# Optimization experiments

Measured on AMD Instinct MI355X. Metric: run time of the kernel, lower is better.

Reference implementation:

```python
import jax, jax.numpy as jnp
import numpy as np
import math

B, S, D, H = 4, 2048, 1024, 16
DK = D // H


def _rope_tables(seq_len, dim, dtype=jnp.float32):
    inv_freq = 1.0 / (10000.0 ** (jnp.arange(0, dim, 2, dtype=jnp.float32) / dim))
    t = jnp.arange(seq_len, dtype=jnp.float32)
    freqs = jnp.einsum('i,j->ij', t, inv_freq)          # [S, dim/2]
    emb = jnp.concatenate([freqs, freqs], axis=-1)       # [S, dim]
    return jnp.cos(emb).astype(dtype)[None, None], jnp.sin(emb).astype(dtype)[None, None]


def _apply_rope(x, cos, sin):
    # faithful to source: rotated = cat([-x[...,1::2], x[...,::2]], -1)
    x_rot = jnp.concatenate([-x[..., 1::2], x[..., ::2]], axis=-1)
    return x * cos + x_rot * sin


def setup_inputs() -> dict:
    key = jax.random.key(0)
    ks = jax.random.split(key, 12)
    scale = 1.0 / math.sqrt(D)
    inp = {
        'query': jax.random.normal(ks[0], (B, S, D), jnp.float32),
        'key':   jax.random.normal(ks[1], (B, S, D), jnp.float32),
        'value': jax.random.normal(ks[2], (B, S, D), jnp.float32),
        'mask':  jnp.tril(jnp.ones((S, S), jnp.int32))[None, None],  # causal [1,1,S,S]
        'w_q': jax.random.normal(ks[3], (D, D), jnp.float32) * scale,
        'b_q': jnp.zeros((D,), jnp.float32),
        'w_k': jax.random.normal(ks[4], (D, D), jnp.float32) * scale,
        'b_k': jnp.zeros((D,), jnp.float32),
        'w_v': jax.random.normal(ks[5], (D, D), jnp.float32) * scale,
        'b_v': jnp.zeros((D,), jnp.float32),
        'w_o': jax.random.normal(ks[6], (D, D), jnp.float32) * scale,
        'b_o': jnp.zeros((D,), jnp.float32),
    }
    return inp


def reference(query, key, value, mask, w_q, b_q, w_k, b_k, w_v, b_v, w_o, b_o):
    b, s, _ = query.shape
    # projections (torch Linear: x @ W.T + b), split heads -> [B,H,S,Dk]
    def proj(x, w, bias):
        return (x @ w.T + bias).reshape(b, -1, H, DK).transpose(0, 2, 1, 3)
    Q = proj(query, w_q, b_q)
    K = proj(key, w_k, b_k)
    V = proj(value, w_v, b_v)
    cos, sin = _rope_tables(s, DK, Q.dtype)
    Q = _apply_rope(Q, cos, sin)
    K = _apply_rope(K, cos, sin)
    scores = jnp.einsum('bhqd,bhkd->bhqk', Q, K) / math.sqrt(DK)
    scores = jnp.where(mask == 0, jnp.asarray(-1e9, scores.dtype), scores)
    attn = jax.nn.softmax(scores, axis=-1)
    ctx = jnp.einsum('bhqk,bhkd->bhqd', attn, V)
    ctx = ctx.transpose(0, 2, 1, 3).reshape(b, -1, D)
    return ctx @ w_o.T + b_o
```

## Files before the change

### kernel.cpp

```cpp
#include <hip/hip_runtime.h>
#include <hip/hip_bf16.h>
#include <math.h>

#define B_  4
#define S_  2048
#define D_  1024
#define H_  16
#define DK_ 64
#define M_  (B_ * S_)

typedef short short8 __attribute__((ext_vector_type(8)));
typedef float floatx4 __attribute__((ext_vector_type(4)));

__device__ inline unsigned short f2bf(float x) {
    unsigned u = __float_as_uint(x);
    u = (u + 0x7fff + ((u >> 16) & 1)) >> 16;
    return (unsigned short)u;
}
__device__ inline float bf2f(unsigned short h) {
    return __uint_as_float(((unsigned)h) << 16);
}

__device__ inline unsigned cvt_pk_bf16(float lo, float hi) {
    unsigned r;
    asm("v_cvt_pk_bf16_f32 %0, %1, %2" : "=v"(r) : "v"(lo), "v"(hi));
    return r;
}

template <int K>
__device__ inline float dpp_ror(float x) {
    return __uint_as_float((unsigned)__builtin_amdgcn_update_dpp(
        0, (int)__float_as_uint(x), 0x120 | K, 0xF, 0xF, true));
}
__device__ inline float rowmax16(float x) {
    x = fmaxf(x, dpp_ror<8>(x));
    x = fmaxf(x, dpp_ror<4>(x));
    x = fmaxf(x, dpp_ror<2>(x));
    x = fmaxf(x, dpp_ror<1>(x));
    return x;
}
__device__ inline float rowsum16(float x) {
    x += dpp_ror<8>(x);
    x += dpp_ror<4>(x);
    x += dpp_ror<2>(x);
    x += dpp_ror<1>(x);
    return x;
}

#define GLOAD_LDS16(g, l)                                          \
    __builtin_amdgcn_global_load_lds(                              \
        (const __attribute__((address_space(1))) void*)(g),        \
        (__attribute__((address_space(3))) void*)(l), 16, 0, 0)

__global__ __launch_bounds__(256) void cvt_inputs_kernel(
    const float* __restrict__ q, const float* __restrict__ k,
    const float* __restrict__ v, unsigned short* __restrict__ Ah)
{
    const int z = blockIdx.z;
    const float* src = (z == 0) ? q : (z == 1) ? k : v;
    unsigned short* dst = Ah + (size_t)z * M_ * D_;
    const size_t i = ((size_t)blockIdx.x * 256 + threadIdx.x) * 4;
    float4 f = *(const float4*)(src + i);
    ushort4 o;
    o.x = f2bf(f.x); o.y = f2bf(f.y); o.z = f2bf(f.z); o.w = f2bf(f.w);
    *(ushort4*)(dst + i) = o;
}

__global__ __launch_bounds__(256) void cvt_weights_kernel(
    const float* __restrict__ wq, const float* __restrict__ wk,
    const float* __restrict__ wv, const float* __restrict__ wo,
    unsigned short* __restrict__ Wh, unsigned short* __restrict__ Woh)
{
    const int z = blockIdx.z;
    const float* src = (z == 0) ? wq : (z == 1) ? wk : (z == 2) ? wv : wo;
    unsigned short* dst = (z < 3) ? (Wh + (size_t)z * D_ * D_) : Woh;
    const size_t i = ((size_t)blockIdx.x * 256 + threadIdx.x) * 4;
    float4 f = *(const float4*)(src + i);
    ushort4 o;
    o.x = f2bf(f.x); o.y = f2bf(f.y); o.z = f2bf(f.z); o.w = f2bf(f.w);
    *(ushort4*)(dst + i) = o;
}

template <int MODE>
__global__ __launch_bounds__(256) void gemm_bf16_kernel(
    const unsigned short* __restrict__ Ah, const unsigned short* __restrict__ Wh,
    const float* __restrict__ bq, const float* __restrict__ bk,
    const float* __restrict__ bv, void* __restrict__ outv)
{
    __shared__ __align__(16) unsigned short As[128 * 32];
    __shared__ __align__(16) unsigned short Bs[128 * 32];
    __shared__ __align__(16) unsigned short Ts[MODE == 1 ? 4 * 16 * 68 : 4];

    const int tid  = threadIdx.x;
    const int wave = tid >> 6;
    const int lane = tid & 63;
    const int quad = lane >> 4;
    const int l15  = lane & 15;
    const int z    = (MODE == 1) ? blockIdx.z : 0;
    const int m0   = blockIdx.x * 128;
    const int n0   = blockIdx.y * 128;
    const int wrow = (wave >> 1) * 64;
    const int wcol = (wave & 1) * 64;

    const unsigned short* A = Ah + (size_t)z * M_ * D_;
    const unsigned short* W = Wh + (size_t)z * D_ * D_;

    const int srow   = tid >> 2;
    const int schunk = (tid & 3) * 8;

    floatx4 acc[4][4] = {};

    for (int k0 = 0; k0 < D_; k0 += 32) {
        __syncthreads();
#pragma unroll
        for (int p = 0; p < 2; ++p) {
            const unsigned short* ga =
                A + (size_t)(m0 + p * 64 + srow) * D_ + k0 + schunk;
            GLOAD_LDS16(ga, &As[p * 2048 + wave * 512]);
            const unsigned short* gb =
                W + (size_t)(n0 + p * 64 + srow) * D_ + k0 + schunk;
            GLOAD_LDS16(gb, &Bs[p * 2048 + wave * 512]);
        }
        __syncthreads();

        short8 af[4], bf[4];
#pragma unroll
        for (int i = 0; i < 4; ++i)
            af[i] = *(const short8*)&As[(wrow + i * 16 + l15) * 32 + quad * 8];
#pragma unroll
        for (int j = 0; j < 4; ++j)
            bf[j] = *(const short8*)&Bs[(wcol + j * 16 + l15) * 32 + quad * 8];
#pragma unroll
        for (int i = 0; i < 4; ++i)
#pragma unroll
            for (int j = 0; j < 4; ++j)
                acc[i][j] = __builtin_amdgcn_mfma_f32_16x16x32_bf16(
                    af[i], bf[j], acc[i][j], 0, 0, 0);
    }

    const float* bias = (MODE == 0) ? bq : (z == 0) ? bq : (z == 1) ? bk : bv;

    if (MODE == 1 && z == 2) {
        __syncthreads();
        unsigned short* Tw = &Ts[wave * 16 * 68];
        const int bgl = m0 >> 11;
        const int s0g = (m0 & (S_ - 1)) + wrow + quad * 16;
#pragma unroll
        for (int j = 0; j < 4; ++j) {
            const int n = n0 + wcol + j * 16 + l15;
            const float bn = bias[n];
#pragma unroll
            for (int i = 0; i < 4; ++i)
#pragma unroll
                for (int reg = 0; reg < 4; ++reg)
                    Tw[l15 * 68 + i * 16 + quad * 4 + reg] =
                        f2bf(acc[i][j][reg] + bn);
            short8 r0 = *(const short8*)&Tw[l15 * 68 + quad * 16];
            short8 r1 = *(const short8*)&Tw[l15 * 68 + quad * 16 + 8];
            const int h = n >> 6, d = n & 63;
            unsigned short* dp = (unsigned short*)outv + 2 * (size_t)M_ * D_ +
                (((size_t)(bgl * H_ + h)) * DK_ + d) * S_ + s0g;
            *(short8*)(dp) = r0;
            *(short8*)(dp + 8) = r1;
        }
        return;
    }

#pragma unroll
    for (int j = 0; j < 4; ++j) {
        const int n = n0 + wcol + j * 16 + l15;
        const float bn = bias[n];
#pragma unroll
        for (int i = 0; i < 4; ++i) {
#pragma unroll
            for (int reg = 0; reg < 4; ++reg) {
                const int m = m0 + wrow + i * 16 + quad * 4 + reg;
                const float v = acc[i][j][reg] + bn;
                if (MODE == 0) {
                    ((float*)outv)[(size_t)m * D_ + n] = v;
                } else {
                    const int b = m >> 11;
                    const int s = m & (S_ - 1);
                    const int h = n >> 6;
                    const int d = n & 63;
                    unsigned short* dst =
                        (unsigned short*)outv + (size_t)z * M_ * D_;
                    dst[(((size_t)b * H_ + h) * S_ + s) * DK_ + d] = f2bf(v);
                }
            }
        }
    }
}

__global__ __launch_bounds__(256) void rope_kernel(unsigned short* __restrict__ Q,
                                                   unsigned short* __restrict__ K)
{
    const int wave = blockIdx.x * 4 + (threadIdx.x >> 6);
    const int lane = threadIdx.x & 63;
    const int rowsPer = B_ * H_ * S_;

    unsigned short* base = (wave < rowsPer) ? Q : K;
    const int row = (wave < rowsPer) ? wave : wave - rowsPer;
    const int s = row & (S_ - 1);

    unsigned short* p = base + (size_t)row * DK_;
    const float v = bf2f(p[lane]);

    const int j = lane & 31;
    const float inv_freq = 1.0f / powf(10000.0f, (float)(2 * j) / (float)DK_);
    const float ang = (float)s * inv_freq;
    const float c  = cosf(ang);
    const float si = sinf(ang);

    const int partner = (lane < 32) ? (2 * lane + 1) : (2 * (lane - 32));
    const float sign = (lane < 32) ? -1.0f : 1.0f;
    const float pv = __shfl(v, partner);

    p[lane] = f2bf(v * c + sign * pv * si);
}

#define KSTR 72

__global__ __launch_bounds__(256, 3) void attn_kernel(
    const unsigned short* __restrict__ Qh, const unsigned short* __restrict__ Kh,
    const unsigned short* __restrict__ Vt, unsigned short* __restrict__ ctx)
{
    __shared__ __align__(16) unsigned short Ks[2][64 * 64];
    __shared__ __align__(16) unsigned short Vs[2][64 * 64];
    __shared__ __align__(16) short Pw[4][16 * KSTR];

    const int tid  = threadIdx.x;
    const int wave = tid >> 6;
    const int lane = tid & 63;
    const int quad = lane >> 4;
    const int l15  = lane & 15;

    const int L  = blockIdx.x;
    const int bh = ((L >> 3) & 7) * 8 + (L & 7);
    const int qt = 31 - (L >> 6);
    const int q0 = qt * 64;

    const float c2 = 0.18033688011f;

    const unsigned short* Kbase = Kh + (size_t)bh * S_ * DK_;
    const unsigned short* Vbase = Vt + (size_t)bh * DK_ * S_;
    const int b = bh >> 4, h = bh & 15;

    short* Pme = &Pw[wave][0];

    const unsigned short* Qrow =
        Qh + ((size_t)bh * S_ + q0 + wave * 16 + l15) * DK_;
    short8 aQ[2];
    aQ[0] = *(const short8*)(Qrow + quad * 8);
    aQ[1] = *(const short8*)(Qrow + 32 + quad * 8);

    const int srow = lane >> 3;
    const int sg   = (lane & 7) ^ srow;
    const unsigned short* kSrc = Kbase + (size_t)(wave * 8 + srow) * DK_ + sg * 8;
    const unsigned short* vSrc = Vbase + (size_t)(wave * 8 + srow) * S_ + sg * 8;

    floatx4 acc[4] = {};
    float m_i[4] = {-INFINITY, -INFINITY, -INFINITY, -INFINITY};
    float l_i[4] = {0.f, 0.f, 0.f, 0.f};

#pragma unroll
    for (int rd = 0; rd < 2; ++rd) {
        GLOAD_LDS16(kSrc + (size_t)rd * 32 * DK_, &Ks[0][rd * 2048 + wave * 512]);
        GLOAD_LDS16(vSrc + (size_t)rd * 32 * S_,  &Vs[0][rd * 2048 + wave * 512]);
    }
    __syncthreads();

    int buf = 0;
    for (int j0 = 0; j0 <= q0; j0 += 64) {
        if (j0 + 64 <= q0) {
#pragma unroll
            for (int rd = 0; rd < 2; ++rd) {
                GLOAD_LDS16(kSrc + (size_t)(j0 + 64 + rd * 32) * DK_,
                            &Ks[buf ^ 1][rd * 2048 + wave * 512]);
                GLOAD_LDS16(vSrc + (j0 + 64) + (size_t)rd * 32 * S_,
                            &Vs[buf ^ 1][rd * 2048 + wave * 512]);
            }
        }

        floatx4 st[4] = {};
#pragma unroll
        for (int t = 0; t < 4; ++t)
#pragma unroll
            for (int kh = 0; kh < 2; ++kh) {
                short8 kf = *(const short8*)&Ks[buf][(t * 16 + l15) * 64 +
                              ((((kh << 2) + quad) ^ (l15 & 7)) << 3)];
                st[t] = __builtin_amdgcn_mfma_f32_16x16x32_bf16(
                    aQ[kh], kf, st[t], 0, 0, 0);
            }

        if (j0 == q0) {
#pragma unroll
            for (int t = 0; t < 4; ++t)
#pragma unroll
                for (int reg = 0; reg < 4; ++reg)
                    if (t * 16 + l15 > wave * 16 + quad * 4 + reg)
                        st[t][reg] = -INFINITY;
        }

#pragma unroll
        for (int reg = 0; reg < 4; ++reg) {
            float rmx = fmaxf(fmaxf(st[0][reg], st[1][reg]),
                              fmaxf(st[2][reg], st[3][reg]));
            rmx = rowmax16(rmx);
            const float m2 = fmaxf(m_i[reg], rmx * c2);
            const float alpha = exp2f(m_i[reg] - m2);

            const float p0 = exp2f(fmaf(st[0][reg], c2, -m2));
            const float p1 = exp2f(fmaf(st[1][reg], c2, -m2));
            const float p2 = exp2f(fmaf(st[2][reg], c2, -m2));
            const float p3 = exp2f(fmaf(st[3][reg], c2, -m2));

            const unsigned pk01 = cvt_pk_bf16(p0, p1);
            const unsigned pk23 = cvt_pk_bf16(p2, p3);
            const int rbase = (quad * 4 + reg) * KSTR + l15;
            Pme[rbase]      = (short)(unsigned short)pk01;
            Pme[rbase + 16] = (short)(unsigned short)(pk01 >> 16);
            Pme[rbase + 32] = (short)(unsigned short)pk23;
            Pme[rbase + 48] = (short)(unsigned short)(pk23 >> 16);

            float rs = (p0 + p1) + (p2 + p3);
            rs = rowsum16(rs);
            l_i[reg] = l_i[reg] * alpha + rs;
            m_i[reg] = m2;
            if (__ballot(alpha == 1.0f) != ~0ull) {
#pragma unroll
                for (int t = 0; t < 4; ++t) acc[t][reg] *= alpha;
            }
        }

#pragma unroll
        for (int kh = 0; kh < 2; ++kh) {
            short8 aP = *(const short8*)&Pme[l15 * KSTR + kh * 32 + quad * 8];
#pragma unroll
            for (int t = 0; t < 4; ++t) {
                short8 vf = *(const short8*)&Vs[buf][(t * 16 + l15) * 64 +
                              ((((kh << 2) + quad) ^ (l15 & 7)) << 3)];
                acc[t] = __builtin_amdgcn_mfma_f32_16x16x32_bf16(
                    aP, vf, acc[t], 0, 0, 0);
            }
        }

        __syncthreads();
        buf ^= 1;
    }

#pragma unroll
    for (int reg = 0; reg < 4; ++reg) {
        const float inv = 1.0f / l_i[reg];
        const int q = q0 + wave * 16 + quad * 4 + reg;
        unsigned short* orow = ctx + ((size_t)b * S_ + q) * D_ + h * DK_;
#pragma unroll
        for (int t = 0; t < 4; ++t)
            orow[t * 16 + l15] = f2bf(acc[t][reg] * inv);
    }
}

extern "C" void kernel_launch(void* const* d_in, const int* in_sizes, int n_in,
                              void* d_out, int out_size, void* d_ws, size_t ws_size,
                              hipStream_t stream)
{
    const float* query = (const float*)d_in[0];
    const float* key   = (const float*)d_in[1];
    const float* value = (const float*)d_in[2];
    const float* w_q = (const float*)d_in[4];
    const float* b_q = (const float*)d_in[5];
    const float* w_k = (const float*)d_in[6];
    const float* b_k = (const float*)d_in[7];
    const float* w_v = (const float*)d_in[8];
    const float* b_v = (const float*)d_in[9];
    const float* w_o = (const float*)d_in[10];
    const float* b_o = (const float*)d_in[11];
    float* out = (float*)d_out;

    char* ws = (char*)d_ws;
    const size_t half = (size_t)M_ * D_ * sizeof(unsigned short);
    unsigned short* Ah   = (unsigned short*)(ws);
    unsigned short* Wh   = (unsigned short*)(ws + 3 * half);
    unsigned short* Woh  = (unsigned short*)(ws + 3 * half + 3 * half / 8);
    unsigned short* QKVb = (unsigned short*)(ws + 3 * half + 4 * half / 8);
    unsigned short* Ctxh = (unsigned short*)(ws + 6 * half + 4 * half / 8);

    cvt_inputs_kernel<<<dim3(M_ * D_ / 1024, 1, 3), 256, 0, stream>>>(
        query, key, value, Ah);
    cvt_weights_kernel<<<dim3(D_ * D_ / 1024, 1, 4), 256, 0, stream>>>(
        w_q, w_k, w_v, w_o, Wh, Woh);

    gemm_bf16_kernel<1><<<dim3(M_ / 128, D_ / 128, 3), 256, 0, stream>>>(
        Ah, Wh, b_q, b_k, b_v, QKVb);

    unsigned short* Qb = QKVb;
    unsigned short* Kb = QKVb + (size_t)M_ * D_;
    unsigned short* Vb = QKVb + 2 * (size_t)M_ * D_;

    rope_kernel<<<(2 * B_ * H_ * S_) / 4, 256, 0, stream>>>(Qb, Kb);

    attn_kernel<<<dim3(2048), 256, 0, stream>>>(Qb, Kb, Vb, Ctxh);

    gemm_bf16_kernel<0><<<dim3(M_ / 128, D_ / 128, 1), 256, 0, stream>>>(
        Ctxh, Woh, b_o, b_o, b_o, out);
}
```

Baseline: 438.3 us.

## Double-buffer GEMM LDS staging, vectorize Q/K epilogue, add lazy softmax rescale

The projection GEMM now double-buffers its A/B LDS tiles. The next K-slice is prefetched while MFMAs run on the current one, leaving a single barrier per iteration. The Q/K epilogue now transposes through LDS (reusing the A buffer) and writes 16-byte vectors instead of scattered 2-byte stores. The attention softmax now skips the running-max update and rescale unless some row's max grows by more than 8 in log2 units. This relies on bounded growth of un-rescaled exponentials, which risks fp32/bf16 range issues.

```diff
diff --git a/kernel.cpp b/kernel.cpp
--- a/kernel.cpp
+++ b/kernel.cpp
@@ -87,9 +87,8 @@
     const float* __restrict__ bq, const float* __restrict__ bk,
     const float* __restrict__ bv, void* __restrict__ outv)
 {
-    __shared__ __align__(16) unsigned short As[128 * 32];
-    __shared__ __align__(16) unsigned short Bs[128 * 32];
-    __shared__ __align__(16) unsigned short Ts[MODE == 1 ? 4 * 16 * 68 : 4];
+    __shared__ __align__(16) unsigned short As[2][128 * 32];
+    __shared__ __align__(16) unsigned short Bs[2][128 * 32];
 
     const int tid  = threadIdx.x;
     const int wave = tid >> 6;
@@ -108,60 +107,93 @@
     const int srow   = tid >> 2;
     const int schunk = (tid & 3) * 8;
 
+#define STAGE_G(BUF, K0)                                                     \
+    {                                                                        \
+        GLOAD_LDS16(A + (size_t)(m0 + srow) * D_ + (K0) + schunk,            \
+                    &As[BUF][wave * 512]);                                   \
+        GLOAD_LDS16(W + (size_t)(n0 + srow) * D_ + (K0) + schunk,            \
+                    &Bs[BUF][wave * 512]);                                   \
+        GLOAD_LDS16(A + (size_t)(m0 + 64 + srow) * D_ + (K0) + schunk,       \
+                    &As[BUF][2048 + wave * 512]);                            \
+        GLOAD_LDS16(W + (size_t)(n0 + 64 + srow) * D_ + (K0) + schunk,       \
+                    &Bs[BUF][2048 + wave * 512]);                            \
+    }
+
     floatx4 acc[4][4] = {};
 
+    STAGE_G(0, 0);
+    __syncthreads();
+
     for (int k0 = 0; k0 < D_; k0 += 32) {
-        __syncthreads();
-#pragma unroll
-        for (int p = 0; p < 2; ++p) {
-            const unsigned short* ga =
-                A + (size_t)(m0 + p * 64 + srow) * D_ + k0 + schunk;
-            GLOAD_LDS16(ga, &As[p * 2048 + wave * 512]);
-            const unsigned short* gb =
-                W + (size_t)(n0 + p * 64 + srow) * D_ + k0 + schunk;
-            GLOAD_LDS16(gb, &Bs[p * 2048 + wave * 512]);
-        }
-        __syncthreads();
+        const int cur = (k0 >> 5) & 1;
+        if (k0 + 32 < D_) STAGE_G(cur ^ 1, k0 + 32);
 
         short8 af[4], bf[4];
 #pragma unroll
         for (int i = 0; i < 4; ++i)
-            af[i] = *(const short8*)&As[(wrow + i * 16 + l15) * 32 + quad * 8];
+            af[i] = *(const short8*)&As[cur][(wrow + i * 16 + l15) * 32 + quad * 8];
 #pragma unroll
         for (int j = 0; j < 4; ++j)
-            bf[j] = *(const short8*)&Bs[(wcol + j * 16 + l15) * 32 + quad * 8];
+            bf[j] = *(const short8*)&Bs[cur][(wcol + j * 16 + l15) * 32 + quad * 8];
 #pragma unroll
         for (int i = 0; i < 4; ++i)
 #pragma unroll
             for (int j = 0; j < 4; ++j)
                 acc[i][j] = __builtin_amdgcn_mfma_f32_16x16x32_bf16(
                     af[i], bf[j], acc[i][j], 0, 0, 0);
-    }
+
+        __syncthreads();
+    }
+#undef STAGE_G
 
     const float* bias = (MODE == 0) ? bq : (z == 0) ? bq : (z == 1) ? bk : bv;
 
-    if (MODE == 1 && z == 2) {
-        __syncthreads();
-        unsigned short* Tw = &Ts[wave * 16 * 68];
-        const int bgl = m0 >> 11;
-        const int s0g = (m0 & (S_ - 1)) + wrow + quad * 16;
-#pragma unroll
-        for (int j = 0; j < 4; ++j) {
-            const int n = n0 + wcol + j * 16 + l15;
-            const float bn = bias[n];
-#pragma unroll
-            for (int i = 0; i < 4; ++i)
-#pragma unroll
-                for (int reg = 0; reg < 4; ++reg)
-                    Tw[l15 * 68 + i * 16 + quad * 4 + reg] =
-                        f2bf(acc[i][j][reg] + bn);
-            short8 r0 = *(const short8*)&Tw[l15 * 68 + quad * 16];
-            short8 r1 = *(const short8*)&Tw[l15 * 68 + quad * 16 + 8];
-            const int h = n >> 6, d = n & 63;
-            unsigned short* dp = (unsigned short*)outv + 2 * (size_t)M_ * D_ +
-                (((size_t)(bgl * H_ + h)) * DK_ + d) * S_ + s0g;
-            *(short8*)(dp) = r0;
-            *(short8*)(dp + 8) = r1;
+    if (MODE == 1) {
+        unsigned short* Tw = (unsigned short*)As + wave * 16 * 68;
+        const int bg = m0 >> 11;
+
+        if (z == 2) {
+            const int s0g = (m0 & (S_ - 1)) + wrow + quad * 16;
+#pragma unroll
+            for (int j = 0; j < 4; ++j) {
+                const int n = n0 + wcol + j * 16 + l15;
+                const float bn = bias[n];
+#pragma unroll
+                for (int i = 0; i < 4; ++i)
+#pragma unroll
+                    for (int reg = 0; reg < 4; ++reg)
+                        Tw[l15 * 68 + i * 16 + quad * 4 + reg] =
+                            f2bf(acc[i][j][reg] + bn);
+                short8 r0 = *(const short8*)&Tw[l15 * 68 + quad * 16];
+                short8 r1 = *(const short8*)&Tw[l15 * 68 + quad * 16 + 8];
+                const int h = n >> 6, d = n & 63;
+                unsigned short* dp = (unsigned short*)outv + 2 * (size_t)M_ * D_ +
+                    (((size_t)(bg * H_ + h)) * DK_ + d) * S_ + s0g;
+                *(short8*)(dp) = r0;
+                *(short8*)(dp + 8) = r1;
+            }
+        } else {
+            const int hq = (n0 + wcol) >> 6;
+            const int sb = (m0 & (S_ - 1)) + wrow;
+            unsigned short* dstz = (unsigned short*)outv + (size_t)z * M_ * D_;
+#pragma unroll
+            for (int i = 0; i < 4; ++i) {
+#pragma unroll
+                for (int j = 0; j < 4; ++j) {
+                    const float bn = bias[n0 + wcol + j * 16 + l15];
+#pragma unroll
+                    for (int reg = 0; reg < 4; ++reg)
+                        Tw[(quad * 4 + reg) * 68 + j * 16 + l15] =
+                            f2bf(acc[i][j][reg] + bn);
+                }
+                short8 r0 = *(const short8*)&Tw[l15 * 68 + quad * 16];
+                short8 r1 = *(const short8*)&Tw[l15 * 68 + quad * 16 + 8];
+                unsigned short* dp = dstz +
+                    (((size_t)bg * H_ + hq) * S_ + sb + i * 16 + l15) * DK_ +
+                    quad * 16;
+                *(short8*)dp = r0;
+                *(short8*)(dp + 8) = r1;
+            }
         }
         return;
     }
@@ -175,18 +207,7 @@
 #pragma unroll
             for (int reg = 0; reg < 4; ++reg) {
                 const int m = m0 + wrow + i * 16 + quad * 4 + reg;
-                const float v = acc[i][j][reg] + bn;
-                if (MODE == 0) {
-                    ((float*)outv)[(size_t)m * D_ + n] = v;
-                } else {
-                    const int b = m >> 11;
-                    const int s = m & (S_ - 1);
-                    const int h = n >> 6;
-                    const int d = n & 63;
-                    unsigned short* dst =
-                        (unsigned short*)outv + (size_t)z * M_ * D_;
-                    dst[(((size_t)b * H_ + h) * S_ + s) * DK_ + d] = f2bf(v);
-                }
+                ((float*)outv)[(size_t)m * D_ + n] = acc[i][j][reg] + bn;
             }
         }
     }
@@ -307,13 +328,23 @@
             float rmx = fmaxf(fmaxf(st[0][reg], st[1][reg]),
                               fmaxf(st[2][reg], st[3][reg]));
             rmx = rowmax16(rmx);
-            const float m2 = fmaxf(m_i[reg], rmx * c2);
-            const float alpha = exp2f(m_i[reg] - m2);
-
-            const float p0 = exp2f(fmaf(st[0][reg], c2, -m2));
-            const float p1 = exp2f(fmaf(st[1][reg], c2, -m2));
-            const float p2 = exp2f(fmaf(st[2][reg], c2, -m2));
-            const float p3 = exp2f(fmaf(st[3][reg], c2, -m2));
+            const float pm = rmx * c2;
+            if (__ballot(pm > m_i[reg] + 8.0f) != 0ull) {
+                const float m2 = fmaxf(m_i[reg], pm);
+                const float alpha = exp2f(m_i[reg] - m2);
+                l_i[reg] *= alpha;
+                m_i[reg] = m2;
+                if (__ballot(alpha == 1.0f) != ~0ull) {
+#pragma unroll
+                    for (int t = 0; t < 4; ++t) acc[t][reg] *= alpha;
+                }
+            }
+            const float m2v = m_i[reg];
+
+            const float p0 = exp2f(fmaf(st[0][reg], c2, -m2v));
+            const float p1 = exp2f(fmaf(st[1][reg], c2, -m2v));
+            const float p2 = exp2f(fmaf(st[2][reg], c2, -m2v));
+            const float p3 = exp2f(fmaf(st[3][reg], c2, -m2v));
 
             const unsigned pk01 = cvt_pk_bf16(p0, p1);
             const unsigned pk23 = cvt_pk_bf16(p2, p3);
@@ -325,12 +356,7 @@
 
             float rs = (p0 + p1) + (p2 + p3);
             rs = rowsum16(rs);
-            l_i[reg] = l_i[reg] * alpha + rs;
-            m_i[reg] = m2;
-            if (__ballot(alpha == 1.0f) != ~0ull) {
-#pragma unroll
-                for (int t = 0; t < 4; ++t) acc[t][reg] *= alpha;
-            }
+            l_i[reg] += rs;
         }
 
 #pragma unroll
```

After: 447.1 us. 1.02x slower.
